# Performance work log

Hardware: AMD Instinct MI355X
Metric: run time of the kernel (lower is better)

Reference implementation:

```python
import jax, jax.numpy as jnp
import numpy as np

B, L, NB = 8192, 40, 2        # batch, maxlen, behavior features
V, E = 100000, 64             # vocab per table, embed dim per table
NS, ND = 3, 8                 # other sparse feats, dense feats
D = NB * E                    # concatenated behavior embed dim = 128
ALL = D + D + (ND + NS * E)   # info_all dim = 456
NEG_INF = -2.0**32 + 1
BN_EPS = 1e-3                 # keras BatchNormalization default epsilon


def setup_inputs() -> dict:
    key = jax.random.key(0)
    ks = jax.random.split(key, 20)
    inp = {
        "dense_inputs": jax.random.normal(ks[0], (B, ND), jnp.float32),
        "sparse_inputs": jax.random.randint(ks[1], (B, NS), 0, V),
        "seq_inputs": jax.random.randint(ks[2], (B, L, NB), 0, V),
        "item_inputs": jax.random.randint(ks[3], (B, NB), 0, V),
        # embedding tables (random_uniform init in keras)
        "emb_sparse": jax.random.uniform(ks[4], (NS, V, E), jnp.float32, -0.05, 0.05),
        "emb_seq": jax.random.uniform(ks[5], (NB, V, E), jnp.float32, -0.05, 0.05),
        # attention MLP: input 4*D=512 -> 80 -> 40 -> 1
        "att_W1": jax.random.normal(ks[6], (4 * D, 80), jnp.float32) * 0.05,
        "att_b1": jnp.zeros((80,), jnp.float32),
        "att_W2": jax.random.normal(ks[7], (80, 40), jnp.float32) * 0.05,
        "att_b2": jnp.zeros((40,), jnp.float32),
        "att_Wf": jax.random.normal(ks[8], (40, 1), jnp.float32) * 0.05,
        "att_bf": jnp.zeros((1,), jnp.float32),
        # batch norm (inference-mode moving stats)
        "bn_gamma": jnp.ones((ALL,), jnp.float32),
        "bn_beta": jnp.zeros((ALL,), jnp.float32),
        "bn_mean": jnp.zeros((ALL,), jnp.float32),
        "bn_var": jnp.ones((ALL,), jnp.float32),
        # FFN: ALL -> 80 -> 40 -> 1, PReLU alphas per-feature
        "ffn_W1": jax.random.normal(ks[9], (ALL, 80), jnp.float32) * 0.05,
        "ffn_b1": jnp.zeros((80,), jnp.float32),
        "ffn_a1": jnp.full((80,), 0.25, jnp.float32),
        "ffn_W2": jax.random.normal(ks[10], (80, 40), jnp.float32) * 0.05,
        "ffn_b2": jnp.zeros((40,), jnp.float32),
        "ffn_a2": jnp.full((40,), 0.25, jnp.float32),
        "out_W": jax.random.normal(ks[11], (40, 1), jnp.float32) * 0.05,
        "out_b": jnp.zeros((1,), jnp.float32),
    }
    return inp


def prelu(x, alpha):
    return jnp.where(x > 0, x, alpha * x)


def reference(dense_inputs, sparse_inputs, seq_inputs, item_inputs,
              emb_sparse, emb_seq,
              att_W1, att_b1, att_W2, att_b2, att_Wf, att_bf,
              bn_gamma, bn_beta, bn_mean, bn_var,
              ffn_W1, ffn_b1, ffn_a1, ffn_W2, ffn_b2, ffn_a2,
              out_W, out_b):
    mask = (seq_inputs[:, :, 0] != 0)                                   # [B, L]
    # other sparse embeddings + dense features
    other_info = jnp.concatenate(
        [dense_inputs] + [emb_sparse[i][sparse_inputs[:, i]] for i in range(NS)], axis=-1)
    # behavior sequence / candidate item embeddings
    seq_embed = jnp.concatenate([emb_seq[i][seq_inputs[:, :, i]] for i in range(NB)], axis=-1)  # [B,L,D]
    item_embed = jnp.concatenate([emb_seq[i][item_inputs[:, i]] for i in range(NB)], axis=-1)   # [B,D]

    # local activation attention
    q = jnp.broadcast_to(item_embed[:, None, :], seq_embed.shape)       # [B,L,D]
    info = jnp.concatenate([q, seq_embed, q - seq_embed, q * seq_embed], axis=-1)  # [B,L,4D]
    h = jax.nn.sigmoid(info @ att_W1 + att_b1)
    h = jax.nn.sigmoid(h @ att_W2 + att_b2)
    logits = (h @ att_Wf + att_bf)[..., 0]                               # [B,L]
    logits = jnp.where(mask, logits, NEG_INF)
    att = jax.nn.softmax(logits, axis=-1)                                # [B,L]
    user_info = jnp.einsum('bl,bld->bd', att, seq_embed)                 # [B,D]

    info_all = jnp.concatenate([user_info, item_embed, other_info], axis=-1)  # [B,ALL]
    info_all = bn_gamma * (info_all - bn_mean) * jax.lax.rsqrt(bn_var + BN_EPS) + bn_beta
    info_all = prelu(info_all @ ffn_W1 + ffn_b1, ffn_a1)
    info_all = prelu(info_all @ ffn_W2 + ffn_b2, ffn_a2)
    return jax.nn.sigmoid(info_all @ out_W + out_b)                      # [B,1]
```

## Files before the change

### kernel.cpp

```cpp
#include <hip/hip_runtime.h>

#define BB 8192
#define LL 40
#define VV 100000
#define NEG_INF_F (-4294967295.0f)
#define XS 136
#define HS 104
#define XGS 480

typedef __attribute__((ext_vector_type(8))) short short8;
typedef __attribute__((ext_vector_type(4))) float f32x4;

__device__ __forceinline__ unsigned cvt_pk_bf16(float a, float b) {
  unsigned r;
  asm("v_cvt_pk_bf16_f32 %0, %1, %2" : "=v"(r) : "v"(a), "v"(b));
  return r;
}
__device__ __forceinline__ unsigned short f2bf(float f) {
  return (unsigned short)cvt_pk_bf16(f, f);
}
__device__ __forceinline__ float bf2f(unsigned short s) {
  return __uint_as_float(((unsigned)s) << 16);
}
__device__ __forceinline__ float sigm(float z) {
  return __builtin_amdgcn_rcpf(1.f + __expf(-z));
}

__device__ __forceinline__ short8 fuseB(short8 wsd, short8 wd, float4 qa, float4 qb) {
  float qv[8] = {qa.x, qa.y, qa.z, qa.w, qb.x, qb.y, qb.z, qb.w};
  float f[8];
#pragma unroll
  for (int j = 0; j < 8; j++)
    f[j] = bf2f((unsigned short)wsd[j]) + qv[j] * bf2f((unsigned short)wd[j]);
  uint4 o;
  o.x = cvt_pk_bf16(f[0], f[1]);
  o.y = cvt_pk_bf16(f[2], f[3]);
  o.z = cvt_pk_bf16(f[4], f[5]);
  o.w = cvt_pk_bf16(f[6], f[7]);
  return __builtin_bit_cast(short8, o);
}

__global__ void prep_all(const float* __restrict__ W1, float* __restrict__ wqcT,
                         unsigned short* __restrict__ WsdpT,
                         const float* __restrict__ aW2, unsigned short* __restrict__ W2bT,
                         const float* __restrict__ fW2, unsigned short* __restrict__ W2fT,
                         const float* __restrict__ fW1, const float* __restrict__ g,
                         const float* __restrict__ vr, unsigned short* __restrict__ W1fT,
                         const float* __restrict__ fb1, const float* __restrict__ be,
                         const float* __restrict__ mn, float* __restrict__ b1p) {
  __shared__ float red[4];
  int bid = blockIdx.x, t = threadIdx.x;
  if (bid < 40) {
    int i = bid * 256 + t;
    int h = i >> 7, k = i & 127;
    float a = W1[k * 80 + h];
    float b = W1[(128 + k) * 80 + h];
    float c = W1[(256 + k) * 80 + h];
    float d = W1[(384 + k) * 80 + h];
    wqcT[h * 132 + k] = a + c;
    WsdpT[h * 256 + k] = f2bf(b - c);
    WsdpT[h * 256 + 128 + k] = f2bf(d);
  } else if (bid < 58) {
    int i = (bid - 40) * 256 + t;
    int n = i / 96, k = i % 96;
    W2bT[i] = (n < 40 && k < 80) ? f2bf(aW2[k * 40 + n]) : (unsigned short)0;
  } else if (bid < 76) {
    int i = (bid - 58) * 256 + t;
    int n = i / 96, k = i % 96;
    W2fT[i] = (n < 40 && k < 80) ? f2bf(fW2[k * 40 + n]) : (unsigned short)0;
  } else if (bid < 226) {
    int i = (bid - 76) * 256 + t;
    int n = i / 480, k = i % 480;
    float v = 0.f;
    if (k < 456) v = fW1[k * 80 + n] * g[k] * rsqrtf(vr[k] + 1e-3f);
    W1fT[i] = f2bf(v);
  } else {
    int n = bid - 226;
    float p = 0.f;
    for (int k = t; k < 456; k += 256) {
      float sc = g[k] * rsqrtf(vr[k] + 1e-3f);
      p += (be[k] - mn[k] * sc) * fW1[k * 80 + n];
    }
    for (int off = 32; off; off >>= 1) p += __shfl_xor(p, off, 64);
    if ((t & 63) == 0) red[t >> 6] = p;
    __syncthreads();
    if (t == 0) b1p[n] = fb1[n] + red[0] + red[1] + red[2] + red[3];
  }
}


__launch_bounds__(256, 8)
__global__ void din_att(const float* __restrict__ dense, const int* __restrict__ sparsei,
                        const int* __restrict__ seqi, const int* __restrict__ itemi,
                        const float* __restrict__ embS, const float* __restrict__ embQ,
                        const float* __restrict__ wqcT, const unsigned short* __restrict__ WsdpT,
                        const unsigned short* __restrict__ W2bT,
                        const float* __restrict__ ab1, const float* __restrict__ ab2,
                        const float* __restrict__ aWf, const float* __restrict__ abf,
                        unsigned short* __restrict__ Xg) {
  __shared__ __align__(16) char smem[20352];
  unsigned short* sX  = (unsigned short*)smem;
  unsigned short* sH1 = (unsigned short*)(smem + 10880);
  float* sQ    = (float*)(smem + 19200);
  float* sQCp  = sQ + 128;
  float* sLA   = sQCp + 80;
  float* sMask = sLA + 40;

  const int t = threadIdx.x;
  const int b = blockIdx.x;
  const int wv = t >> 6, ln = t & 63, m16 = ln & 15, quad = ln >> 4;
  unsigned short* xrow = Xg + (size_t)b * XGS;

  if (t < 32) {
    int f = t >> 4, sub = t & 15;
    int idx = itemi[b * 2 + f];
    float4 v = *(const float4*)(embQ + ((size_t)(f * VV + idx)) * 64 + sub * 4);
    *(float4*)(sQ + f * 64 + sub * 4) = v;
    uint2 p;
    p.x = cvt_pk_bf16(v.x, v.y);
    p.y = cvt_pk_bf16(v.z, v.w);
    *(uint2*)(xrow + 128 + f * 64 + sub * 4) = p;
  } else if (t < 80) {
    int j = t - 32, f = j >> 4, sub = j & 15;
    int idx = sparsei[b * 3 + f];
    float4 v = *(const float4*)(embS + ((size_t)(f * VV + idx)) * 64 + sub * 4);
    uint2 p;
    p.x = cvt_pk_bf16(v.x, v.y);
    p.y = cvt_pk_bf16(v.z, v.w);
    *(uint2*)(xrow + 264 + f * 64 + sub * 4) = p;
  } else if (t < 88) {
    xrow[256 + (t - 80)] = f2bf(dense[b * 8 + (t - 80)]);
  } else if (t < 100) {
    ((unsigned*)xrow)[228 + (t - 88)] = 0u;
  } else if (t < 140) {
    sLA[t - 100] = 0.f;
  }
  for (int i = t; i < 1280; i += 256) {
    int r = i >> 4, sub = i & 15;
    int l = r >> 1, f = r & 1;
    int idx = seqi[b * 80 + r];
    float4 v = *(const float4*)(embQ + ((size_t)(f * VV + idx)) * 64 + sub * 4);
    uint2 p;
    p.x = cvt_pk_bf16(v.x, v.y);
    p.y = cvt_pk_bf16(v.z, v.w);
    *(uint2*)(sX + l * XS + f * 64 + sub * 4) = p;
    if (((r & 1) | sub) == 0) sMask[l] = (idx != 0) ? 0.f : NEG_INF_F;
  }
  for (int i = t; i < 320; i += 256) {
    int r = i >> 3, c = i & 7;
    ((unsigned*)sH1)[r * 52 + 40 + c] = 0u;
  }
  __syncthreads();

  if (t < 80) {
    float acc0 = ab1[t], acc1 = 0.f;
    const float* wq = wqcT + t * 132;
    for (int k = 0; k < 128; k += 8) {
      float4 w0 = *(const float4*)(wq + k);
      float4 w1 = *(const float4*)(wq + k + 4);
      float4 q0 = *(const float4*)(sQ + k);
      float4 q1 = *(const float4*)(sQ + k + 4);
      acc0 += q0.x * w0.x + q0.y * w0.y + q0.z * w0.z + q0.w * w0.w;
      acc1 += q1.x * w1.x + q1.y * w1.y + q1.z * w1.z + q1.w * w1.w;
    }
    sQCp[t] = acc0 + acc1;
  }
  short8 Bp[4];
  {
    const unsigned short* br = WsdpT + (size_t)(wv * 16 + m16) * 256 + quad * 8;
#pragma unroll
    for (int kt = 0; kt < 4; kt++) {
      short8 w1 = *(const short8*)(br + kt * 32);
      short8 w2 = *(const short8*)(br + 128 + kt * 32);
      int k0 = quad * 8 + kt * 32;
      Bp[kt] = fuseB(w1, w2, *(const float4*)(sQ + k0), *(const float4*)(sQ + k0 + 4));
    }
  }
  __syncthreads();

  {
    const int h = wv * 16 + m16;
    const float qc = sQCp[h];
#pragma unroll
    for (int mt = 0; mt < 3; mt++) {
      f32x4 acc = {0.f, 0.f, 0.f, 0.f};
      const unsigned short* ar = sX + (mt * 16 + m16) * XS + quad * 8;
#pragma unroll
      for (int kt = 0; kt < 4; kt++) {
        short8 a = *(const short8*)(ar + kt * 32);
        acc = __builtin_amdgcn_mfma_f32_16x16x32_bf16(a, Bp[kt], acc, 0, 0, 0);
      }
      float s0 = sigm(acc[0] + qc), s1 = sigm(acc[1] + qc);
      float s2 = sigm(acc[2] + qc), s3 = sigm(acc[3] + qc);
      unsigned p01 = cvt_pk_bf16(s0, s1), p23 = cvt_pk_bf16(s2, s3);
      int l0 = mt * 16 + quad * 4;
      if (l0 < 40) {
        sH1[(l0 + 0) * HS + h] = (unsigned short)p01;
        sH1[(l0 + 1) * HS + h] = (unsigned short)(p01 >> 16);
        sH1[(l0 + 2) * HS + h] = (unsigned short)p23;
        sH1[(l0 + 3) * HS + h] = (unsigned short)(p23 >> 16);
      }
    }
    if (wv < 3) {
      const unsigned short* br = WsdpT + (size_t)(64 + m16) * 256 + quad * 8;
      const unsigned short* ar = sX + (wv * 16 + m16) * XS + quad * 8;
      f32x4 acc = {0.f, 0.f, 0.f, 0.f};
#pragma unroll
      for (int kt = 0; kt < 4; kt++) {
        short8 w1 = *(const short8*)(br + kt * 32);
        short8 w2 = *(const short8*)(br + 128 + kt * 32);
        int k0 = quad * 8 + kt * 32;
        short8 bp = fuseB(w1, w2, *(const float4*)(sQ + k0), *(const float4*)(sQ + k0 + 4));
        short8 a = *(const short8*)(ar + kt * 32);
        acc = __builtin_amdgcn_mfma_f32_16x16x32_bf16(a, bp, acc, 0, 0, 0);
      }
      int h4 = 64 + m16;
      float qc4 = sQCp[h4];
      float s0 = sigm(acc[0] + qc4), s1 = sigm(acc[1] + qc4);
      float s2 = sigm(acc[2] + qc4), s3 = sigm(acc[3] + qc4);
      unsigned p01 = cvt_pk_bf16(s0, s1), p23 = cvt_pk_bf16(s2, s3);
      int l0 = wv * 16 + quad * 4;
      if (l0 < 40) {
        sH1[(l0 + 0) * HS + h4] = (unsigned short)p01;
        sH1[(l0 + 1) * HS + h4] = (unsigned short)(p01 >> 16);
        sH1[(l0 + 2) * HS + h4] = (unsigned short)p23;
        sH1[(l0 + 3) * HS + h4] = (unsigned short)(p23 >> 16);
      }
    }
  }
  __syncthreads();

  for (int tile = wv; tile < 9; tile += 4) {
    int mt = tile / 3, nt = tile % 3;
    f32x4 acc = {0.f, 0.f, 0.f, 0.f};
    int arow = mt * 16 + m16;
    if (arow > 39) arow = 39;
    const unsigned short* ar = sH1 + arow * HS + quad * 8;
    const unsigned short* br = W2bT + (nt * 16 + m16) * 96 + quad * 8;
#pragma unroll
    for (int kt = 0; kt < 3; kt++) {
      short8 a = *(const short8*)(ar + kt * 32);
      short8 bb = *(const short8*)(br + kt * 32);
      acc = __builtin_amdgcn_mfma_f32_16x16x32_bf16(a, bb, acc, 0, 0, 0);
    }
    int j = nt * 16 + m16;
    float b2 = (j < 40) ? ab2[j] : 0.f;
    float wf = (j < 40) ? aWf[j] : 0.f;
    float c[4];
#pragma unroll
    for (int r = 0; r < 4; r++) {
      float h2 = sigm(acc[r] + b2);
      c[r] = (j < 40) ? h2 * wf : 0.f;
    }
#pragma unroll
    for (int off = 1; off < 16; off <<= 1) {
#pragma unroll
      for (int r = 0; r < 4; r++) c[r] += __shfl_xor(c[r], off, 64);
    }
    if (m16 == 0) {
#pragma unroll
      for (int r = 0; r < 4; r++) {
        int l = mt * 16 + quad * 4 + r;
        if (l < 40) atomicAdd(&sLA[l], c[r]);
      }
    }
  }
  __syncthreads();

  if (wv == 0) {
    float logit = -3.0e38f;
    if (t < 40) logit = sLA[t] + abf[0] + sMask[t];
    float mx = logit;
    for (int off = 32; off; off >>= 1) mx = fmaxf(mx, __shfl_xor(mx, off, 64));
    float ex = (t < 40) ? __expf(logit - mx) : 0.f;
    float sm = ex;
    for (int off = 32; off; off >>= 1) sm += __shfl_xor(sm, off, 64);
    if (t < 40) sLA[t] = ex * __builtin_amdgcn_rcpf(sm);
  }
  __syncthreads();

  if (t < 128) {
    float acc = 0.f;
    for (int l = 0; l < 40; l++) acc += sLA[l] * bf2f(sX[l * XS + t]);
    xrow[t] = f2bf(acc);
  }
}


__launch_bounds__(256, 2)
__global__ void din_ffn(const unsigned short* __restrict__ Xg,
                        const unsigned short* __restrict__ W1fT, const float* __restrict__ b1p,
                        const float* __restrict__ fa1,
                        const unsigned short* __restrict__ W2fT, const float* __restrict__ fb2,
                        const float* __restrict__ fa2,
                        const float* __restrict__ oW, const float* __restrict__ ob,
                        float* __restrict__ out) {
  __shared__ __align__(16) unsigned short sXB[16 * 488];
  __shared__ __align__(16) unsigned short sH1B[16 * HS];
  __shared__ float sH2B[16 * 41];
  const int t = threadIdx.x, blk = blockIdx.x;
  const int wv = t >> 6, ln = t & 63, m16 = ln & 15, quad = ln >> 4;

  short8 Bf[15];
  {
    const unsigned short* br = W1fT + (size_t)(wv * 16 + m16) * 480 + quad * 8;
#pragma unroll
    for (int kt = 0; kt < 15; kt++) Bf[kt] = *(const short8*)(br + kt * 32);
  }

  for (int i = t; i < 960; i += 256) {
    int r = i / 60, c = i % 60;
    *(uint4*)(sXB + r * 488 + c * 8) =
        *(const uint4*)(Xg + (size_t)(blk * 16 + r) * XGS + c * 8);
  }
  if (t < 128) {
    int r = t >> 3, c = t & 7;
    ((unsigned*)sH1B)[r * 52 + 40 + c] = 0u;
  }
  __syncthreads();

  {
    int h = wv * 16 + m16;
    f32x4 acc = {0.f, 0.f, 0.f, 0.f};
    const unsigned short* ar = sXB + m16 * 488 + quad * 8;
#pragma unroll
    for (int kt = 0; kt < 15; kt++) {
      short8 a = *(const short8*)(ar + kt * 32);
      acc = __builtin_amdgcn_mfma_f32_16x16x32_bf16(a, Bf[kt], acc, 0, 0, 0);
    }
    float b1v = b1p[h], a1v = fa1[h];
    float z0 = acc[0] + b1v, z1 = acc[1] + b1v, z2 = acc[2] + b1v, z3 = acc[3] + b1v;
    z0 = z0 > 0.f ? z0 : a1v * z0;
    z1 = z1 > 0.f ? z1 : a1v * z1;
    z2 = z2 > 0.f ? z2 : a1v * z2;
    z3 = z3 > 0.f ? z3 : a1v * z3;
    unsigned p01 = cvt_pk_bf16(z0, z1), p23 = cvt_pk_bf16(z2, z3);
    int l0 = quad * 4;
    sH1B[(l0 + 0) * HS + h] = (unsigned short)p01;
    sH1B[(l0 + 1) * HS + h] = (unsigned short)(p01 >> 16);
    sH1B[(l0 + 2) * HS + h] = (unsigned short)p23;
    sH1B[(l0 + 3) * HS + h] = (unsigned short)(p23 >> 16);
    if (wv == 0) {
      short8 B4[15];
      const unsigned short* br = W1fT + (size_t)(64 + m16) * 480 + quad * 8;
#pragma unroll
      for (int kt = 0; kt < 15; kt++) B4[kt] = *(const short8*)(br + kt * 32);
      f32x4 acc4 = {0.f, 0.f, 0.f, 0.f};
#pragma unroll
      for (int kt = 0; kt < 15; kt++) {
        short8 a = *(const short8*)(ar + kt * 32);
        acc4 = __builtin_amdgcn_mfma_f32_16x16x32_bf16(a, B4[kt], acc4, 0, 0, 0);
      }
      int h4 = 64 + m16;
      float b1v4 = b1p[h4], a1v4 = fa1[h4];
      float y0 = acc4[0] + b1v4, y1 = acc4[1] + b1v4, y2 = acc4[2] + b1v4, y3 = acc4[3] + b1v4;
      y0 = y0 > 0.f ? y0 : a1v4 * y0;
      y1 = y1 > 0.f ? y1 : a1v4 * y1;
      y2 = y2 > 0.f ? y2 : a1v4 * y2;
      y3 = y3 > 0.f ? y3 : a1v4 * y3;
      unsigned q01 = cvt_pk_bf16(y0, y1), q23 = cvt_pk_bf16(y2, y3);
      sH1B[(l0 + 0) * HS + h4] = (unsigned short)q01;
      sH1B[(l0 + 1) * HS + h4] = (unsigned short)(q01 >> 16);
      sH1B[(l0 + 2) * HS + h4] = (unsigned short)q23;
      sH1B[(l0 + 3) * HS + h4] = (unsigned short)(q23 >> 16);
    }
  }
  __syncthreads();

  if (wv < 3) {
    f32x4 acc = {0.f, 0.f, 0.f, 0.f};
    const unsigned short* ar = sH1B + m16 * HS + quad * 8;
    const unsigned short* br = W2fT + (wv * 16 + m16) * 96 + quad * 8;
#pragma unroll
    for (int kt = 0; kt < 3; kt++) {
      short8 a = *(const short8*)(ar + kt * 32);
      short8 bb = *(const short8*)(br + kt * 32);
      acc = __builtin_amdgcn_mfma_f32_16x16x32_bf16(a, bb, acc, 0, 0, 0);
    }
    int j = wv * 16 + m16;
    if (j < 40) {
      float b2 = fb2[j], a2 = fa2[j];
#pragma unroll
      for (int r = 0; r < 4; r++) {
        int l = quad * 4 + r;
        float z = acc[r] + b2;
        sH2B[l * 41 + j] = z > 0.f ? z : a2 * z;
      }
    }
  }
  __syncthreads();

  if (t < 16) {
    float acc = ob[0];
    for (int j = 0; j < 40; j++) acc += sH2B[t * 41 + j] * oW[j];
    out[blk * 16 + t] = sigm(acc);
  }
}


extern "C" void kernel_launch(void* const* d_in, const int* in_sizes, int n_in,
                              void* d_out, int out_size, void* d_ws, size_t ws_size,
                              hipStream_t stream) {
  const float* dense  = (const float*)d_in[0];
  const int*   sparsei = (const int*)d_in[1];
  const int*   seqi   = (const int*)d_in[2];
  const int*   itemi  = (const int*)d_in[3];
  const float* embS   = (const float*)d_in[4];
  const float* embQ   = (const float*)d_in[5];
  const float* aW1    = (const float*)d_in[6];
  const float* ab1    = (const float*)d_in[7];
  const float* aW2    = (const float*)d_in[8];
  const float* ab2    = (const float*)d_in[9];
  const float* aWf    = (const float*)d_in[10];
  const float* abf    = (const float*)d_in[11];
  const float* bng    = (const float*)d_in[12];
  const float* bnb    = (const float*)d_in[13];
  const float* bnm    = (const float*)d_in[14];
  const float* bnv    = (const float*)d_in[15];
  const float* fW1    = (const float*)d_in[16];
  const float* fb1    = (const float*)d_in[17];
  const float* fa1    = (const float*)d_in[18];
  const float* fW2    = (const float*)d_in[19];
  const float* fb2    = (const float*)d_in[20];
  const float* fa2    = (const float*)d_in[21];
  const float* oW     = (const float*)d_in[22];
  const float* ob     = (const float*)d_in[23];
  float* out = (float*)d_out;

  float* ws = (float*)d_ws;
  float* wqcT = ws;
  float* b1p  = ws + 10560;
  unsigned short* WsdpT = (unsigned short*)(ws + 10640);
  unsigned short* W2bT  = (unsigned short*)(ws + 20880);
  unsigned short* W2fT  = (unsigned short*)(ws + 23184);
  unsigned short* W1fT  = (unsigned short*)(ws + 25488);
  unsigned short* Xg    = (unsigned short*)(ws + 44688);

  prep_all<<<306, 256, 0, stream>>>(aW1, wqcT, WsdpT, aW2, W2bT, fW2, W2fT,
                                    fW1, bng, bnv, W1fT, fb1, bnb, bnm, b1p);
  din_att<<<BB, 256, 0, stream>>>(dense, sparsei, seqi, itemi, embS, embQ,
                                  wqcT, WsdpT, W2bT, ab1, ab2, aWf, abf, Xg);
  din_ffn<<<512, 256, 0, stream>>>(Xg, W1fT, b1p, fa1, W2fT, fb2, fa2, oW, ob, out);
}
```

Before: 320.8 us.

## Pre-convert behavior embedding table to bf16 and prefetch gathers into registers

Each call, prep_all now converts the whole behavior embedding table to bf16 in workspace when there is room. The attention kernel then gathers half-width rows, issuing those gathers into registers early so their latency overlaps the query projection and B-fragment setup. The softmax and weighted sum are split across two waves with a private attention vector, which removes one block barrier. The trade is a full-table read and write in every call, which only pays off if it is cheaper than the fp32 random-gather traffic it removes.

```diff
diff --git a/kernel.cpp b/kernel.cpp
--- a/kernel.cpp
+++ b/kernel.cpp
@@ -47,7 +47,8 @@
                          const float* __restrict__ fW1, const float* __restrict__ g,
                          const float* __restrict__ vr, unsigned short* __restrict__ W1fT,
                          const float* __restrict__ fb1, const float* __restrict__ be,
-                         const float* __restrict__ mn, float* __restrict__ b1p) {
+                         const float* __restrict__ mn, float* __restrict__ b1p,
+                         const float* __restrict__ embQ, unsigned short* __restrict__ embQb) {
   __shared__ float red[4];
   int bid = blockIdx.x, t = threadIdx.x;
   if (bid < 40) {
@@ -74,7 +75,7 @@
     float v = 0.f;
     if (k < 456) v = fW1[k * 80 + n] * g[k] * rsqrtf(vr[k] + 1e-3f);
     W1fT[i] = f2bf(v);
-  } else {
+  } else if (bid < 306) {
     int n = bid - 226;
     float p = 0.f;
     for (int k = t; k < 456; k += 256) {
@@ -85,6 +86,16 @@
     if ((t & 63) == 0) red[t >> 6] = p;
     __syncthreads();
     if (t == 0) b1p[n] = fb1[n] + red[0] + red[1] + red[2] + red[3];
+  } else {
+    const float4* src = (const float4*)embQ;
+    uint2* dst = (uint2*)embQb;
+    for (int i = (bid - 306) * 256 + t; i < 3200000; i += 2048 * 256) {
+      float4 v = src[i];
+      uint2 p;
+      p.x = cvt_pk_bf16(v.x, v.y);
+      p.y = cvt_pk_bf16(v.z, v.w);
+      dst[i] = p;
+    }
   }
 }
 
@@ -93,6 +104,7 @@
 __global__ void din_att(const float* __restrict__ dense, const int* __restrict__ sparsei,
                         const int* __restrict__ seqi, const int* __restrict__ itemi,
                         const float* __restrict__ embS, const float* __restrict__ embQ,
+                        const unsigned short* __restrict__ embQb,
                         const float* __restrict__ wqcT, const unsigned short* __restrict__ WsdpT,
                         const unsigned short* __restrict__ W2bT,
                         const float* __restrict__ ab1, const float* __restrict__ ab2,
@@ -120,7 +132,30 @@
     p.x = cvt_pk_bf16(v.x, v.y);
     p.y = cvt_pk_bf16(v.z, v.w);
     *(uint2*)(xrow + 128 + f * 64 + sub * 4) = p;
-  } else if (t < 80) {
+  } else if (t >= 100 && t < 140) {
+    sLA[t - 100] = 0.f;
+  }
+  for (int i = t; i < 320; i += 256) {
+    int r = i >> 3, c = i & 7;
+    ((unsigned*)sH1)[r * 52 + 40 + c] = 0u;
+  }
+  __syncthreads();
+
+  uint2 gv[5];
+#pragma unroll
+  for (int it = 0; it < 5; it++) {
+    int i = t + (it << 8);
+    int r = i >> 4, sub = i & 15, f = r & 1;
+    int idx = seqi[b * 80 + r];
+    if (embQb) {
+      gv[it] = *(const uint2*)(embQb + ((size_t)(f * VV + idx)) * 64 + sub * 4);
+    } else {
+      float4 v = *(const float4*)(embQ + ((size_t)(f * VV + idx)) * 64 + sub * 4);
+      gv[it].x = cvt_pk_bf16(v.x, v.y);
+      gv[it].y = cvt_pk_bf16(v.z, v.w);
+    }
+  }
+  if (t >= 32 && t < 80) {
     int j = t - 32, f = j >> 4, sub = j & 15;
     int idx = sparsei[b * 3 + f];
     float4 v = *(const float4*)(embS + ((size_t)(f * VV + idx)) * 64 + sub * 4);
@@ -128,30 +163,11 @@
     p.x = cvt_pk_bf16(v.x, v.y);
     p.y = cvt_pk_bf16(v.z, v.w);
     *(uint2*)(xrow + 264 + f * 64 + sub * 4) = p;
-  } else if (t < 88) {
+  } else if (t >= 80 && t < 88) {
     xrow[256 + (t - 80)] = f2bf(dense[b * 8 + (t - 80)]);
-  } else if (t < 100) {
+  } else if (t >= 88 && t < 100) {
     ((unsigned*)xrow)[228 + (t - 88)] = 0u;
-  } else if (t < 140) {
-    sLA[t - 100] = 0.f;
-  }
-  for (int i = t; i < 1280; i += 256) {
-    int r = i >> 4, sub = i & 15;
-    int l = r >> 1, f = r & 1;
-    int idx = seqi[b * 80 + r];
-    float4 v = *(const float4*)(embQ + ((size_t)(f * VV + idx)) * 64 + sub * 4);
-    uint2 p;
-    p.x = cvt_pk_bf16(v.x, v.y);
-    p.y = cvt_pk_bf16(v.z, v.w);
-    *(uint2*)(sX + l * XS + f * 64 + sub * 4) = p;
-    if (((r & 1) | sub) == 0) sMask[l] = (idx != 0) ? 0.f : NEG_INF_F;
-  }
-  for (int i = t; i < 320; i += 256) {
-    int r = i >> 3, c = i & 7;
-    ((unsigned*)sH1)[r * 52 + 40 + c] = 0u;
-  }
-  __syncthreads();
-
+  }
   if (t < 80) {
     float acc0 = ab1[t], acc1 = 0.f;
     const float* wq = wqcT + t * 132;
@@ -174,6 +190,19 @@
       short8 w2 = *(const short8*)(br + 128 + kt * 32);
       int k0 = quad * 8 + kt * 32;
       Bp[kt] = fuseB(w1, w2, *(const float4*)(sQ + k0), *(const float4*)(sQ + k0 + 4));
+    }
+  }
+#pragma unroll
+  for (int it = 0; it < 5; it++) {
+    int i = t + (it << 8);
+    int r = i >> 4, sub = i & 15, l = r >> 1, f = r & 1;
+    *(uint2*)(sX + l * XS + f * 64 + sub * 4) = gv[it];
+  }
+  if ((t & 31) == 0) {
+#pragma unroll
+    for (int it = 0; it < 5; it++) {
+      int r = (t >> 4) + (it << 4);
+      sMask[r >> 1] = (seqi[b * 80 + r] != 0) ? 0.f : NEG_INF_F;
     }
   }
   __syncthreads();
@@ -267,21 +296,18 @@
   }
   __syncthreads();
 
-  if (wv == 0) {
+  if (wv < 2) {
     float logit = -3.0e38f;
-    if (t < 40) logit = sLA[t] + abf[0] + sMask[t];
+    if (ln < 40) logit = sLA[ln] + abf[0] + sMask[ln];
     float mx = logit;
     for (int off = 32; off; off >>= 1) mx = fmaxf(mx, __shfl_xor(mx, off, 64));
-    float ex = (t < 40) ? __expf(logit - mx) : 0.f;
+    float ex = (ln < 40) ? __expf(logit - mx) : 0.f;
     float sm = ex;
     for (int off = 32; off; off >>= 1) sm += __shfl_xor(sm, off, 64);
-    if (t < 40) sLA[t] = ex * __builtin_amdgcn_rcpf(sm);
-  }
-  __syncthreads();
-
-  if (t < 128) {
+    float* av = sQCp + wv * 40;
+    if (ln < 40) av[ln] = ex * __builtin_amdgcn_rcpf(sm);
     float acc = 0.f;
-    for (int l = 0; l < 40; l++) acc += sLA[l] * bf2f(sX[l * XS + t]);
+    for (int l = 0; l < 40; l++) acc += av[l] * bf2f(sX[l * XS + t]);
     xrow[t] = f2bf(acc);
   }
 }
@@ -436,9 +462,16 @@
   unsigned short* W1fT  = (unsigned short*)(ws + 25488);
   unsigned short* Xg    = (unsigned short*)(ws + 44688);
 
-  prep_all<<<306, 256, 0, stream>>>(aW1, wqcT, WsdpT, aW2, W2bT, fW2, W2fT,
-                                    fW1, bng, bnv, W1fT, fb1, bnb, bnm, b1p);
-  din_att<<<BB, 256, 0, stream>>>(dense, sparsei, seqi, itemi, embS, embQ,
+  size_t base = 44688ull * 4 + 8192ull * 480 * 2;
+  size_t need = base + 12800000ull * 2;
+  unsigned short* embQb = (ws_size >= need)
+      ? (unsigned short*)((char*)d_ws + base) : (unsigned short*)0;
+
+  int prep_grid = embQb ? 2354 : 306;
+  prep_all<<<prep_grid, 256, 0, stream>>>(aW1, wqcT, WsdpT, aW2, W2bT, fW2, W2fT,
+                                          fW1, bng, bnv, W1fT, fb1, bnb, bnm, b1p,
+                                          embQ, embQb);
+  din_att<<<BB, 256, 0, stream>>>(dense, sparsei, seqi, itemi, embS, embQ, embQb,
                                   wqcT, WsdpT, W2bT, ab1, ab2, aWf, abf, Xg);
   din_ffn<<<512, 256, 0, stream>>>(Xg, W1fT, b1p, fa1, W2fT, fb2, fa2, oW, ob, out);
 }
```

Result: slower. 335.5 us (+4.6%).
